# Kernel optimization log

Hardware: AMD Instinct MI355X
Metric: run time of the kernel (lower is better)

## Reference

```python
import jax, jax.numpy as jnp
import numpy as np

NUM_HEADS = 8
NUM_LEVELS = 4
NUM_POINTS = 16
NUM_BEV = 2
EMBED = 256
BS = 64
NQ = NUM_LEVELS * NUM_POINTS  # 64


def _bilinear_sample(img, grid):
    """F.grid_sample(mode='bilinear', padding_mode='zeros', align_corners=False).
    img: (N, C, H, W); grid: (N, Hg, Wg, 2) in [-1, 1] (x, y). Returns (N, C, Hg, Wg)."""
    N, C, H, W = img.shape
    gx = (grid[..., 0] + 1.0) * (W * 0.5) - 0.5  # (N, Hg, Wg)
    gy = (grid[..., 1] + 1.0) * (H * 0.5) - 0.5
    x0 = jnp.floor(gx)
    y0 = jnp.floor(gy)
    flat = img.reshape(N, C, H * W)

    def gather(xi, yi):
        valid = (xi >= 0) & (xi <= W - 1) & (yi >= 0) & (yi <= H - 1)
        xc = jnp.clip(xi, 0, W - 1).astype(jnp.int32)
        yc = jnp.clip(yi, 0, H - 1).astype(jnp.int32)
        idx = (yc * W + xc).reshape(N, 1, -1)
        g = jnp.take_along_axis(flat, idx, axis=2).reshape(N, C, xi.shape[1], xi.shape[2])
        return g * valid[:, None, :, :].astype(img.dtype)

    wx1 = (gx - x0)[:, None]  # (N,1,Hg,Wg)
    wy1 = (gy - y0)[:, None]
    v00 = gather(x0, y0)
    v01 = gather(x0 + 1.0, y0)
    v10 = gather(x0, y0 + 1.0)
    v11 = gather(x0 + 1.0, y0 + 1.0)
    top = v00 * (1.0 - wx1) + v01 * wx1
    bot = v10 * (1.0 - wx1) + v11 * wx1
    return top * (1.0 - wy1) + bot * wy1


def _forward(query, key_hist, value_hist, reference_points, W_off, b_off, spatial_shapes):
    bs, nq, d = query.shape
    Hn, L, P, BEV = NUM_HEADS, NUM_LEVELS, NUM_POINTS, NUM_BEV
    dh = d // Hn
    Pb = P * BEV
    ss = np.asarray(spatial_shapes)  # (L, 2) static (h, w)

    queries = jnp.concatenate([query, query], axis=1)           # (bs, 2*nq, d)
    keies = jnp.concatenate([query, key_hist], axis=1)
    values = jnp.concatenate([query, value_hist], axis=1)
    qb = queries.shape[1]

    # sampling offsets projection (the only used learned linear in the original forward)
    off = (queries @ W_off + b_off).reshape(bs, qb, Hn, Pb, L, 2)

    # NOTE: original re-assigns q/k/v from the RAW concatenated tensors (to_Q/to_K/to_V discarded)
    qh = queries.reshape(bs, qb, Hn, dh)
    kh = keies.reshape(bs, qb, Hn, dh)
    vh = values.reshape(bs, qb, Hn, dh)

    attn = jax.nn.softmax(jnp.einsum('bqhd,bkhd->bqhk', qh, kh), axis=-1)
    attn = attn.reshape(bs, qb, Hn, L, Pb)

    rp = jnp.concatenate([reference_points, reference_points], axis=1)  # (bs, qb, L, 2)
    norm = jnp.stack([jnp.asarray(ss[:, 1], jnp.float32),
                      jnp.asarray(ss[:, 0], jnp.float32)], axis=-1)      # (L, 2) = (w, h)
    loc = rp[:, :, None, None, :, :] + off / norm                        # (bs,qb,H,Pb,L,2)
    # FAITHFUL: original uses .view here (pure reshape, not a transpose)
    loc = loc.reshape(bs, qb, Hn, L, Pb, 2)
    grids = 2.0 * loc - 1.0

    sampled = []
    start = 0
    for l in range(L):
        h_, w_ = int(ss[l, 0]), int(ss[l, 1])
        vl = vh[:, start:start + h_ * w_]                                # (bs, hw, H, dh)
        start += h_ * w_
        img = vl.transpose(0, 2, 3, 1).reshape(bs * Hn, dh, h_, w_)      # (bs*H, dh, h, w)
        grid_l = grids[:, :, :, l].transpose(0, 2, 1, 3, 4).reshape(bs * Hn, qb, Pb, 2)
        sampled.append(_bilinear_sample(img, grid_l))                    # (bs*H, dh, qb, Pb)

    samp = jnp.stack(sampled, axis=-2).reshape(bs * Hn, dh, qb, L * Pb)
    aw = attn.transpose(0, 2, 1, 3, 4).reshape(bs * Hn, 1, qb, L * Pb)
    out = (samp * aw).sum(-1)                                            # (bs*H, dh, qb)
    # FAITHFUL: original reshapes q_bev dim as (nq, BEV) and means over BEV
    out = out.reshape(bs, Hn * dh, nq, BEV).mean(-1).transpose(0, 2, 1)  # (bs, nq, d)
    return out + query  # dropout is identity at eval


def setup_inputs() -> dict:
    key = jax.random.key(0)
    ks = jax.random.split(key, 6)
    query = jax.random.normal(ks[0], (BS, NQ, EMBED), jnp.float32)
    key_hist = jax.random.normal(ks[1], (BS, NQ, EMBED), jnp.float32)
    value_hist = jax.random.normal(ks[2], (BS, NQ, EMBED), jnp.float32)
    reference_points = jax.random.uniform(ks[3], (BS, NQ, NUM_LEVELS, 2), jnp.float32)
    spatial_shapes = jnp.array([[4, 8]] * NUM_LEVELS, dtype=jnp.int32)  # sum(h*w)=128=L*P*BEV
    off_dim = NUM_HEADS * NUM_BEV * NUM_POINTS * NUM_LEVELS * 2
    W_off = jax.random.normal(ks[4], (EMBED, off_dim), jnp.float32) * 0.02
    b_off = jnp.zeros((off_dim,), jnp.float32)
    return {"query": query, "key_hist": key_hist, "value_hist": value_hist,
            "reference_points": reference_points, "spatial_shapes": spatial_shapes,
            "W_off": W_off, "b_off": b_off}


def reference(query, key_hist, value_hist, reference_points, spatial_shapes, W_off, b_off):
    return _forward(query, key_hist, value_hist, reference_points, W_off, b_off, spatial_shapes)
```

## Files before the change

kernel.cpp:

```cpp
#include <hip/hip_runtime.h>


typedef short  s16x8 __attribute__((ext_vector_type(8)));
typedef float  f32x4 __attribute__((ext_vector_type(4)));

__device__ __forceinline__ unsigned short f2bf(float f) {
    union { float f; unsigned u; } v; v.f = f;
    unsigned r = v.u + 0x7FFFu + ((v.u >> 16) & 1u);
    return (unsigned short)(r >> 16);
}
__device__ __forceinline__ float bf2f(unsigned short u) {
    return __uint_as_float(((unsigned)u) << 16);
}
__device__ __forceinline__ s16x8 pack8(const float4 a, const float4 b) {
    s16x8 o;
    o[0] = (short)f2bf(a.x); o[1] = (short)f2bf(a.y);
    o[2] = (short)f2bf(a.z); o[3] = (short)f2bf(a.w);
    o[4] = (short)f2bf(b.x); o[5] = (short)f2bf(b.y);
    o[6] = (short)f2bf(b.z); o[7] = (short)f2bf(b.w);
    return o;
}

__global__ __launch_bounds__(256, 2) void mega3(
    const float* __restrict__ query, const float* __restrict__ key_hist,
    const float* __restrict__ value_hist, const float* __restrict__ refp,
    const float* __restrict__ W, const float* __restrict__ bias,
    float* __restrict__ out)
{
    const int h = blockIdx.x, b = blockIdx.y;
    const int t = threadIdx.x, lane = t & 63, wave = t >> 6;
    const int quad = lane >> 4, col = lane & 15;
    const int wq = wave * 16;

    __shared__ __align__(16) short VTl[32 * 136];
    __shared__ __align__(16) short attLb[64 * 136];
    __shared__ __align__(16) float rpsL[512];
    __shared__ __align__(16) float AmU[8448];
    float* Am  = AmU;
    short* Amb = (short*)AmU;

    {
        #pragma unroll
        for (int u = 0; u < 33; ++u) AmU[t + 256 * u] = 0.f;
    }
    {
        const int p = t >> 1, hf = (t & 1) * 16;
        const float* src = ((p < 64) ? query : value_hist) +
                           (size_t)(b * 64 + (p & 63)) * 256 + h * 32 + hf;
        #pragma unroll
        for (int u = 0; u < 4; ++u) {
            const float4 v = *(const float4*)(src + 4 * u);
            VTl[(hf + 4 * u + 0) * 136 + p] = (short)f2bf(v.x);
            VTl[(hf + 4 * u + 1) * 136 + p] = (short)f2bf(v.y);
            VTl[(hf + 4 * u + 2) * 136 + p] = (short)f2bf(v.z);
            VTl[(hf + 4 * u + 3) * 136 + p] = (short)f2bf(v.w);
        }
    }
    rpsL[t]       = refp[(size_t)b * 512 + t];
    rpsL[t + 256] = refp[(size_t)b * 512 + t + 256];

    {
        const float* qp = query + ((size_t)b * 64 + wq + col) * 256 + h * 32 + quad * 8;
        const s16x8 aq = pack8(*(const float4*)qp, *(const float4*)(qp + 4));
        f32x4 lacc[8];
        #pragma unroll
        for (int t8 = 0; t8 < 8; ++t8) {
            const float* kp = ((t8 < 4)
                ? (query    + ((size_t)b * 64 + 16 * t8 + col) * 256)
                : (key_hist + ((size_t)b * 64 + 16 * (t8 - 4) + col) * 256))
                + h * 32 + quad * 8;
            const s16x8 bk = pack8(*(const float4*)kp, *(const float4*)(kp + 4));
            const f32x4 z = {0.f, 0.f, 0.f, 0.f};
            lacc[t8] = __builtin_amdgcn_mfma_f32_16x16x32_bf16(aq, bk, z, 0, 0, 0);
        }
        #pragma unroll
        for (int r = 0; r < 4; ++r) {
            float m = lacc[0][r];
            #pragma unroll
            for (int t8 = 1; t8 < 8; ++t8) m = fmaxf(m, lacc[t8][r]);
            #pragma unroll
            for (int s = 1; s < 16; s <<= 1) m = fmaxf(m, __shfl_xor(m, s, 64));
            float e[8], ssum = 0.f;
            #pragma unroll
            for (int t8 = 0; t8 < 8; ++t8) {
                e[t8] = __expf(lacc[t8][r] - m); ssum += e[t8];
            }
            #pragma unroll
            for (int s = 1; s < 16; s <<= 1) ssum += __shfl_xor(ssum, s, 64);
            const float inv = 1.0f / ssum;
            const int q = wq + 4 * quad + r;
            #pragma unroll
            for (int t8 = 0; t8 < 8; ++t8)
                attLb[q * 136 + 16 * t8 + col] = (short)f2bf(e[t8] * inv);
        }
    }

    f32x4 acc[4][4] = {};
    {
        const int nbase = h * 256 + wave * 64;
        #pragma unroll
        for (int kq = 0; kq < 4; ++kq) {
            #pragma unroll
            for (int ks = 0; ks < 2; ++ks) {
                const int k0 = kq * 64 + ks * 32 + quad * 8;
                s16x8 af[4];
                #pragma unroll
                for (int mi = 0; mi < 4; ++mi) {
                    const float* ap = query + ((size_t)b * 64 + 16 * mi + col) * 256 + k0;
                    af[mi] = pack8(*(const float4*)ap, *(const float4*)(ap + 4));
                }
                #pragma unroll
                for (int nj = 0; nj < 4; ++nj) {
                    const float* wp = W + (size_t)k0 * 2048 + nbase + 16 * nj + col;
                    s16x8 bfv;
                    #pragma unroll
                    for (int j = 0; j < 8; ++j)
                        bfv[j] = (short)f2bf(wp[(size_t)j * 2048]);
                    #pragma unroll
                    for (int mi = 0; mi < 4; ++mi)
                        acc[mi][nj] = __builtin_amdgcn_mfma_f32_16x16x32_bf16(
                            af[mi], bfv, acc[mi][nj], 0, 0, 0);
                }
            }
        }
    }
    __syncthreads();

    {
        const int i   = col >> 1;
        const int par = col & 1;
        const int base = 32 * wave;
        #pragma unroll
        for (int nj = 0; nj < 4; ++nj) {
            const float bj = bias[h * 256 + wave * 64 + 16 * nj + col];
            const int f = 32 * wave + 8 * nj + i;
            #pragma unroll
            for (int mi = 0; mi < 4; ++mi) {
                float v[4], p[4];
                #pragma unroll
                for (int r = 0; r < 4; ++r) v[r] = acc[mi][nj][r] + bj;
                #pragma unroll
                for (int r = 0; r < 4; ++r) p[r] = __shfl_xor(v[r], 1, 64);
                #pragma unroll
                for (int rs = 0; rs < 2; ++rs) {
                    const int r = par * 2 + rs;
                    const float ox = par ? p[r] : v[r];
                    const float oy = par ? v[r] : p[r];
                    const int q = 16 * mi + 4 * quad + r;
                    const float2 rp = *(const float2*)&rpsL[q * 8 + (i & 3) * 2];
                    const float a = bf2f((unsigned short)attLb[q * 136 + f]);
                    const float gx = 8.f * (rp.x + ox * 0.125f) - 0.5f;
                    const float gy = 4.f * (rp.y + oy * 0.25f) - 0.5f;
                    const float x0f = floorf(gx), y0f = floorf(gy);
                    const float wx = gx - x0f, wy = gy - y0f;
                    const int x0 = (int)x0f, y0 = (int)y0f;
                    float* rowW = &Am[q * 132 + base];
                    const bool xv0 = (x0 >= 0) && (x0 < 8);
                    const bool xv1 = (x0 >= -1) && (x0 < 7);
                    const bool yv0 = (y0 >= 0) && (y0 < 4);
                    const bool yv1 = (y0 >= -1) && (y0 < 3);
                    if (xv0 && yv0) unsafeAtomicAdd(&rowW[y0 * 8 + x0],           a * (1.f - wx) * (1.f - wy));
                    if (xv1 && yv0) unsafeAtomicAdd(&rowW[y0 * 8 + x0 + 1],       a * wx * (1.f - wy));
                    if (xv0 && yv1) unsafeAtomicAdd(&rowW[(y0 + 1) * 8 + x0],     a * (1.f - wx) * wy);
                    if (xv1 && yv1) unsafeAtomicAdd(&rowW[(y0 + 1) * 8 + x0 + 1], a * wx * wy);
                }
            }
        }
    }
    __syncthreads();

    {
        const int cq = t >> 2, cc = (t & 3) * 32;
        float vreg[32];
        #pragma unroll
        for (int u = 0; u < 8; ++u) {
            const float4 v = *(const float4*)&Am[cq * 132 + cc + 4 * u];
            vreg[4 * u + 0] = v.x; vreg[4 * u + 1] = v.y;
            vreg[4 * u + 2] = v.z; vreg[4 * u + 3] = v.w;
        }
        __syncthreads();
        #pragma unroll
        for (int u = 0; u < 4; ++u) {
            s16x8 o;
            #pragma unroll
            for (int j = 0; j < 8; ++j) o[j] = (short)f2bf(vreg[u * 8 + j]);
            *(s16x8*)&Amb[cq * 136 + cc + u * 8] = o;
        }
    }
    __syncthreads();
    {
        f32x4 oacc[2] = {};
        #pragma unroll
        for (int ks = 0; ks < 4; ++ks) {
            const s16x8 af = *(const s16x8*)&Amb[(wq + col) * 136 + ks * 32 + quad * 8];
            #pragma unroll
            for (int n2 = 0; n2 < 2; ++n2) {
                const s16x8 bv = *(const s16x8*)&VTl[(n2 * 16 + col) * 136
                                                     + ks * 32 + quad * 8];
                oacc[n2] = __builtin_amdgcn_mfma_f32_16x16x32_bf16(af, bv, oacc[n2], 0, 0, 0);
            }
        }
        #pragma unroll
        for (int n2 = 0; n2 < 2; ++n2) {
            const int d = h * 32 + n2 * 16 + col;
            #pragma unroll
            for (int pr = 0; pr < 2; ++pr) {
                const float avg = 0.5f * (oacc[n2][2 * pr] + oacc[n2][2 * pr + 1]);
                const int pj = wave * 8 + quad * 2 + pr;
                const size_t re = ((size_t)b * 64 + pj) * 256 + d;
                const size_t ro = ((size_t)b * 64 + pj + 32) * 256 + d;
                out[re] = query[re] + avg;
                out[ro] = query[ro] + avg;
            }
        }
    }
}

extern "C" void kernel_launch(void* const* d_in, const int* in_sizes, int n_in,
                              void* d_out, int out_size, void* d_ws, size_t ws_size,
                              hipStream_t stream) {
    (void)in_sizes; (void)n_in; (void)out_size; (void)d_ws; (void)ws_size;
    const float* query      = (const float*)d_in[0];
    const float* key_hist   = (const float*)d_in[1];
    const float* value_hist = (const float*)d_in[2];
    const float* refp       = (const float*)d_in[3];
    const float* W_off      = (const float*)d_in[5];
    const float* b_off      = (const float*)d_in[6];
    float* out = (float*)d_out;

    mega3<<<dim3(8, 64), 256, 0, stream>>>(query, key_hist, value_hist,
                                           refp, W_off, b_off, out);
}
```

Baseline: 165.7 us.

## Split each head-batch block across two query halves to double grid parallelism

Adds a grid z dimension so each block handles 32 of the 64 queries, halving shared memory, accumulators and per-block work, and raises launch_bounds occupancy to 4 blocks per CU. The goal is better latency hiding and CU fill, since the original 512-block grid gives relatively few waves per CU on a large GPU. The cost is duplicated work per block: the V transpose and the W_off column loads are repeated by both halves, and waves 2-3 compute attention logits they then discard.

Measured after the change: 166.4 us. No clear change (+0.5%).

```diff
diff --git a/kernel.cpp b/kernel.cpp
--- a/kernel.cpp
+++ b/kernel.cpp
@@ -21,27 +21,31 @@
     return o;
 }
 
-__global__ __launch_bounds__(256, 2) void mega3(
+__global__ __launch_bounds__(256, 4) void mega4(
     const float* __restrict__ query, const float* __restrict__ key_hist,
     const float* __restrict__ value_hist, const float* __restrict__ refp,
     const float* __restrict__ W, const float* __restrict__ bias,
     float* __restrict__ out)
 {
-    const int h = blockIdx.x, b = blockIdx.y;
+    const int h = blockIdx.x, b = blockIdx.y, s = blockIdx.z;
+    const int q0 = s * 32;
     const int t = threadIdx.x, lane = t & 63, wave = t >> 6;
     const int quad = lane >> 4, col = lane & 15;
-    const int wq = wave * 16;
+    const int mw = wave & 1;
 
     __shared__ __align__(16) short VTl[32 * 136];
-    __shared__ __align__(16) short attLb[64 * 136];
-    __shared__ __align__(16) float rpsL[512];
-    __shared__ __align__(16) float AmU[8448];
+    __shared__ __align__(16) short attLb[32 * 136];
+    __shared__ __align__(16) float rpsL[256];
+    __shared__ __align__(16) float AmU[32 * 132];
     float* Am  = AmU;
     short* Amb = (short*)AmU;
 
     {
         #pragma unroll
-        for (int u = 0; u < 33; ++u) AmU[t + 256 * u] = 0.f;
+        for (int u = 0; u < 17; ++u) {
+            const int idx = t + 256 * u;
+            if (idx < 32 * 132) AmU[idx] = 0.f;
+        }
     }
     {
         const int p = t >> 1, hf = (t & 1) * 16;
@@ -56,11 +60,11 @@
             VTl[(hf + 4 * u + 3) * 136 + p] = (short)f2bf(v.w);
         }
     }
-    rpsL[t]       = refp[(size_t)b * 512 + t];
-    rpsL[t + 256] = refp[(size_t)b * 512 + t + 256];
-
-    {
-        const float* qp = query + ((size_t)b * 64 + wq + col) * 256 + h * 32 + quad * 8;
+    rpsL[t & 255] = refp[(size_t)b * 512 + q0 * 8 + (t & 255)];
+
+    {
+        const float* qp = query + ((size_t)b * 64 + q0 + mw * 16 + col) * 256
+                          + h * 32 + quad * 8;
         const s16x8 aq = pack8(*(const float4*)qp, *(const float4*)(qp + 4));
         f32x4 lacc[8];
         #pragma unroll
@@ -73,29 +77,31 @@
             const f32x4 z = {0.f, 0.f, 0.f, 0.f};
             lacc[t8] = __builtin_amdgcn_mfma_f32_16x16x32_bf16(aq, bk, z, 0, 0, 0);
         }
-        #pragma unroll
-        for (int r = 0; r < 4; ++r) {
-            float m = lacc[0][r];
-            #pragma unroll
-            for (int t8 = 1; t8 < 8; ++t8) m = fmaxf(m, lacc[t8][r]);
-            #pragma unroll
-            for (int s = 1; s < 16; s <<= 1) m = fmaxf(m, __shfl_xor(m, s, 64));
-            float e[8], ssum = 0.f;
-            #pragma unroll
-            for (int t8 = 0; t8 < 8; ++t8) {
-                e[t8] = __expf(lacc[t8][r] - m); ssum += e[t8];
+        if (wave < 2) {
+            #pragma unroll
+            for (int r = 0; r < 4; ++r) {
+                float m = lacc[0][r];
+                #pragma unroll
+                for (int t8 = 1; t8 < 8; ++t8) m = fmaxf(m, lacc[t8][r]);
+                #pragma unroll
+                for (int sh = 1; sh < 16; sh <<= 1) m = fmaxf(m, __shfl_xor(m, sh, 64));
+                float e[8], ssum = 0.f;
+                #pragma unroll
+                for (int t8 = 0; t8 < 8; ++t8) {
+                    e[t8] = __expf(lacc[t8][r] - m); ssum += e[t8];
+                }
+                #pragma unroll
+                for (int sh = 1; sh < 16; sh <<= 1) ssum += __shfl_xor(ssum, sh, 64);
+                const float inv = 1.0f / ssum;
+                const int ql = mw * 16 + 4 * quad + r;
+                #pragma unroll
+                for (int t8 = 0; t8 < 8; ++t8)
+                    attLb[ql * 136 + 16 * t8 + col] = (short)f2bf(e[t8] * inv);
             }
-            #pragma unroll
-            for (int s = 1; s < 16; s <<= 1) ssum += __shfl_xor(ssum, s, 64);
-            const float inv = 1.0f / ssum;
-            const int q = wq + 4 * quad + r;
-            #pragma unroll
-            for (int t8 = 0; t8 < 8; ++t8)
-                attLb[q * 136 + 16 * t8 + col] = (short)f2bf(e[t8] * inv);
-        }
-    }
-
-    f32x4 acc[4][4] = {};
+        }
+    }
+
+    f32x4 acc[2][4] = {};
     {
         const int nbase = h * 256 + wave * 64;
         #pragma unroll
@@ -103,10 +109,11 @@
             #pragma unroll
             for (int ks = 0; ks < 2; ++ks) {
                 const int k0 = kq * 64 + ks * 32 + quad * 8;
-                s16x8 af[4];
-                #pragma unroll
-                for (int mi = 0; mi < 4; ++mi) {
-                    const float* ap = query + ((size_t)b * 64 + 16 * mi + col) * 256 + k0;
+                s16x8 af[2];
+                #pragma unroll
+                for (int mi = 0; mi < 2; ++mi) {
+                    const float* ap = query +
+                        ((size_t)b * 64 + q0 + 16 * mi + col) * 256 + k0;
                     af[mi] = pack8(*(const float4*)ap, *(const float4*)(ap + 4));
                 }
                 #pragma unroll
@@ -117,7 +124,7 @@
                     for (int j = 0; j < 8; ++j)
                         bfv[j] = (short)f2bf(wp[(size_t)j * 2048]);
                     #pragma unroll
-                    for (int mi = 0; mi < 4; ++mi)
+                    for (int mi = 0; mi < 2; ++mi)
                         acc[mi][nj] = __builtin_amdgcn_mfma_f32_16x16x32_bf16(
                             af[mi], bfv, acc[mi][nj], 0, 0, 0);
                 }
@@ -135,7 +142,7 @@
             const float bj = bias[h * 256 + wave * 64 + 16 * nj + col];
             const int f = 32 * wave + 8 * nj + i;
             #pragma unroll
-            for (int mi = 0; mi < 4; ++mi) {
+            for (int mi = 0; mi < 2; ++mi) {
                 float v[4], p[4];
                 #pragma unroll
                 for (int r = 0; r < 4; ++r) v[r] = acc[mi][nj][r] + bj;
@@ -146,15 +153,15 @@
                     const int r = par * 2 + rs;
                     const float ox = par ? p[r] : v[r];
                     const float oy = par ? v[r] : p[r];
-                    const int q = 16 * mi + 4 * quad + r;
-                    const float2 rp = *(const float2*)&rpsL[q * 8 + (i & 3) * 2];
-                    const float a = bf2f((unsigned short)attLb[q * 136 + f]);
+                    const int ql = 16 * mi + 4 * quad + r;
+                    const float2 rp = *(const float2*)&rpsL[ql * 8 + (i & 3) * 2];
+                    const float a = bf2f((unsigned short)attLb[ql * 136 + f]);
                     const float gx = 8.f * (rp.x + ox * 0.125f) - 0.5f;
                     const float gy = 4.f * (rp.y + oy * 0.25f) - 0.5f;
                     const float x0f = floorf(gx), y0f = floorf(gy);
                     const float wx = gx - x0f, wy = gy - y0f;
                     const int x0 = (int)x0f, y0 = (int)y0f;
-                    float* rowW = &Am[q * 132 + base];
+                    float* rowW = &Am[ql * 132 + base];
                     const bool xv0 = (x0 >= 0) && (x0 < 8);
                     const bool xv1 = (x0 >= -1) && (x0 < 7);
                     const bool yv0 = (y0 >= 0) && (y0 < 4);
@@ -170,17 +177,17 @@
     __syncthreads();
 
     {
-        const int cq = t >> 2, cc = (t & 3) * 32;
-        float vreg[32];
-        #pragma unroll
-        for (int u = 0; u < 8; ++u) {
+        const int cq = t >> 3, cc = (t & 7) * 16;
+        float vreg[16];
+        #pragma unroll
+        for (int u = 0; u < 4; ++u) {
             const float4 v = *(const float4*)&Am[cq * 132 + cc + 4 * u];
             vreg[4 * u + 0] = v.x; vreg[4 * u + 1] = v.y;
             vreg[4 * u + 2] = v.z; vreg[4 * u + 3] = v.w;
         }
         __syncthreads();
         #pragma unroll
-        for (int u = 0; u < 4; ++u) {
+        for (int u = 0; u < 2; ++u) {
             s16x8 o;
             #pragma unroll
             for (int j = 0; j < 8; ++j) o[j] = (short)f2bf(vreg[u * 8 + j]);
@@ -189,29 +196,25 @@
     }
     __syncthreads();
     {
-        f32x4 oacc[2] = {};
+        const int nt = wave >> 1;
+        f32x4 oacc = {};
         #pragma unroll
         for (int ks = 0; ks < 4; ++ks) {
-            const s16x8 af = *(const s16x8*)&Amb[(wq + col) * 136 + ks * 32 + quad * 8];
-            #pragma unroll
-            for (int n2 = 0; n2 < 2; ++n2) {
-                const s16x8 bv = *(const s16x8*)&VTl[(n2 * 16 + col) * 136
-                                                     + ks * 32 + quad * 8];
-                oacc[n2] = __builtin_amdgcn_mfma_f32_16x16x32_bf16(af, bv, oacc[n2], 0, 0, 0);
-            }
-        }
-        #pragma unroll
-        for (int n2 = 0; n2 < 2; ++n2) {
-            const int d = h * 32 + n2 * 16 + col;
-            #pragma unroll
-            for (int pr = 0; pr < 2; ++pr) {
-                const float avg = 0.5f * (oacc[n2][2 * pr] + oacc[n2][2 * pr + 1]);
-                const int pj = wave * 8 + quad * 2 + pr;
-                const size_t re = ((size_t)b * 64 + pj) * 256 + d;
-                const size_t ro = ((size_t)b * 64 + pj + 32) * 256 + d;
-                out[re] = query[re] + avg;
-                out[ro] = query[ro] + avg;
-            }
+            const s16x8 af = *(const s16x8*)&Amb[(mw * 16 + col) * 136
+                                                 + ks * 32 + quad * 8];
+            const s16x8 bv = *(const s16x8*)&VTl[(nt * 16 + col) * 136
+                                                 + ks * 32 + quad * 8];
+            oacc = __builtin_amdgcn_mfma_f32_16x16x32_bf16(af, bv, oacc, 0, 0, 0);
+        }
+        const int d = h * 32 + nt * 16 + col;
+        #pragma unroll
+        for (int pr = 0; pr < 2; ++pr) {
+            const float avg = 0.5f * (oacc[2 * pr] + oacc[2 * pr + 1]);
+            const int pj = (q0 >> 1) + mw * 8 + quad * 2 + pr;
+            const size_t re = ((size_t)b * 64 + pj) * 256 + d;
+            const size_t ro = ((size_t)b * 64 + pj + 32) * 256 + d;
+            out[re] = query[re] + avg;
+            out[ro] = query[ro] + avg;
         }
     }
 }
@@ -228,6 +231,6 @@
     const float* b_off      = (const float*)d_in[6];
     float* out = (float*)d_out;
 
-    mega3<<<dim3(8, 64), 256, 0, stream>>>(query, key_hist, value_hist,
-                                           refp, W_off, b_off, out);
-}
+    mega4<<<dim3(8, 64, 2), 256, 0, stream>>>(query, key_hist, value_hist,
+                                              refp, W_off, b_off, out);
+}
```
